# Kernel optimization log

Hardware: AMD Instinct MI355X
Metric: run time of the kernel (lower is better)

Reference implementation:

```python
import jax, jax.numpy as jnp
import numpy as np

N_NODES = 50000
N_EDGES = 500000


def setup_inputs() -> dict:
    key = jax.random.key(0)
    ks = jax.random.split(key, 24)
    p = {}
    p['x_feat'] = jax.random.normal(ks[0], (N_NODES, 24), dtype=jnp.float32)
    p['edge_index'] = jax.random.randint(ks[1], (2, N_EDGES), 0, N_NODES)
    p['edge_attr'] = jax.random.uniform(ks[2], (N_EDGES, 16), dtype=jnp.float32)
    def lin(k, fan_in, shape):
        b = 1.0 / np.sqrt(fan_in)
        return jax.random.uniform(k, shape, jnp.float32, -b, b)
    # group-0 input projection: 24 -> 32
    p['lin_prep_W'] = lin(ks[3], 24, (24, 32)); p['lin_prep_b'] = lin(ks[4], 24, (32,))
    # prep tube: 32 -> 16
    p['tube_W'] = lin(ks[5], 32, (32, 16)); p['tube_b'] = lin(ks[6], 32, (16,))
    # shared edge-attr trunk: 16 -> 32 -> 16
    p['edge_W1'] = lin(ks[7], 16, (16, 32)); p['edge_b1'] = lin(ks[8], 16, (32,))
    p['edge_W2'] = lin(ks[9], 32, (32, 16)); p['edge_b2'] = lin(ks[10], 32, (16,))
    # conv1: in=16, out=8 per aggr (mean, max, add)
    p['conv1_edge_W'] = lin(ks[11], 16, (3, 16, 16 * 8)); p['conv1_edge_b'] = lin(ks[12], 16, (3, 16 * 8))
    p['conv1_root_W'] = lin(ks[13], 16, (3, 16, 8)); p['conv1_bias'] = lin(ks[14], 16, (3, 8))
    # conv2: in=24, out=8 per aggr
    p['conv2_edge_W'] = lin(ks[15], 16, (3, 16, 24 * 8)); p['conv2_edge_b'] = lin(ks[16], 16, (3, 24 * 8))
    p['conv2_root_W'] = lin(ks[17], 24, (3, 24, 8)); p['conv2_bias'] = lin(ks[18], 24, (3, 8))
    # output head: 24 -> 2
    p['out_W'] = lin(ks[19], 24, (24, 2)); p['out_b'] = lin(ks[20], 24, (2,))
    return p


def _nnconv(x, e_repr, src, dst, edge_W, edge_b, root_W, bias, n_nodes):
    # x: [N, in]; e_repr: [E, 16]; edge_W: [3, 16, in*out]
    d_in = x.shape[1]
    x_src = x[src]  # [E, in]
    deg = jax.ops.segment_sum(jnp.ones_like(src, dtype=x.dtype), dst, num_segments=n_nodes)  # [N]
    outs = []
    for a, aggr in enumerate(('mean', 'max', 'add')):
        W_e = (e_repr @ edge_W[a] + edge_b[a]).reshape(e_repr.shape[0], d_in, -1)  # [E, in, out]
        msg = jnp.einsum('ei,eio->eo', x_src, W_e)  # [E, out]
        if aggr == 'add':
            agg = jax.ops.segment_sum(msg, dst, num_segments=n_nodes)
        elif aggr == 'mean':
            agg = jax.ops.segment_sum(msg, dst, num_segments=n_nodes) / jnp.maximum(deg, 1.0)[:, None]
        else:
            agg = jax.ops.segment_max(msg, dst, num_segments=n_nodes)
            agg = jnp.where(deg[:, None] > 0, agg, 0.0)  # no-neighbor nodes -> 0
        outs.append(agg + x @ root_W[a] + bias[a])
    return jax.nn.relu(jnp.concatenate(outs, axis=1))  # [N, 3*out]


def reference(x_feat, edge_index, edge_attr, lin_prep_W, lin_prep_b, tube_W, tube_b,
              edge_W1, edge_b1, edge_W2, edge_b2,
              conv1_edge_W, conv1_edge_b, conv1_root_W, conv1_bias,
              conv2_edge_W, conv2_edge_b, conv2_root_W, conv2_bias,
              out_W, out_b):
    n_nodes = x_feat.shape[0]
    src, dst = edge_index[0], edge_index[1]
    # node prep: group projection + tube (relu acts, dropout=0 -> identity)
    x = jax.nn.relu(x_feat @ lin_prep_W + lin_prep_b)       # [N, 32]
    x = jax.nn.relu(x @ tube_W + tube_b)                    # [N, 16]
    # shared edge-attr trunk (last activation = sigmoid), computed once
    e = jax.nn.relu(edge_attr @ edge_W1 + edge_b1)
    e_repr = jax.nn.sigmoid(e @ edge_W2 + edge_b2)          # [E, 16]
    # hop 1 and hop 2 of edge-conditioned NNConv with mean/max/add aggregators
    x = _nnconv(x, e_repr, src, dst, conv1_edge_W, conv1_edge_b, conv1_root_W, conv1_bias, n_nodes)  # [N, 24]
    x = _nnconv(x, e_repr, src, dst, conv2_edge_W, conv2_edge_b, conv2_root_W, conv2_bias, n_nodes)  # [N, 24]
    logits = x @ out_W + out_b                              # [N, 2]
    scores = jax.nn.softmax(logits, axis=1)
    return (logits, scores)
```

## Files before the change

### kernel.cpp

```cpp
#include <hip/hip_runtime.h>

#define BS 256

__device__ __forceinline__ unsigned short f2bf(float f) {
    unsigned x = __float_as_uint(f);
    return (unsigned short)((x + 0x7fffu + ((x >> 16) & 1u)) >> 16);
}
__device__ __forceinline__ void unpack8(uint4 v, float* d) {
    d[0] = __uint_as_float(v.x << 16); d[1] = __uint_as_float(v.x & 0xFFFF0000u);
    d[2] = __uint_as_float(v.y << 16); d[3] = __uint_as_float(v.y & 0xFFFF0000u);
    d[4] = __uint_as_float(v.z << 16); d[5] = __uint_as_float(v.z & 0xFFFF0000u);
    d[6] = __uint_as_float(v.w << 16); d[7] = __uint_as_float(v.w & 0xFFFF0000u);
}
__device__ __forceinline__ uint4 pack8bf(const float* r) {
    unsigned w[4];
#pragma unroll
    for (int j = 0; j < 4; j++)
        w[j] = (unsigned)f2bf(r[2 * j]) | ((unsigned)f2bf(r[2 * j + 1]) << 16);
    return make_uint4(w[0], w[1], w[2], w[3]);
}
__device__ __forceinline__ void st24bf(unsigned short* p, const float* r) {
    uint4* q = (uint4*)p;
    q[0] = pack8bf(r);
    q[1] = pack8bf(r + 8);
    q[2] = pack8bf(r + 16);
}

__global__ void prep_kernel(const float* __restrict__ xf,
                            const float* __restrict__ W1, const float* __restrict__ b1,
                            const float* __restrict__ W2, const float* __restrict__ b2,
                            float* __restrict__ x16, int N)
{
    int n = blockIdx.x * blockDim.x + threadIdx.x;
    bool valid = n < N;
    int nn = valid ? n : 0;
    float a[24];
#pragma unroll
    for (int i = 0; i < 24; i += 4)
        *(float4*)(a + i) = *(const float4*)(xf + (size_t)nn * 24 + i);
    float h[32];
#pragma unroll
    for (int j = 0; j < 32; j++) {
        float s = b1[j];
#pragma unroll
        for (int i = 0; i < 24; i++) s = fmaf(a[i], W1[i * 32 + j], s);
        h[j] = fmaxf(s, 0.f);
    }
    if (!valid) return;
#pragma unroll
    for (int j = 0; j < 16; j++) {
        float s = b2[j];
#pragma unroll
        for (int i = 0; i < 32; i++) s = fmaf(h[i], W2[i * 16 + j], s);
        x16[(size_t)n * 16 + j] = fmaxf(s, 0.f);
    }
}

__global__ void degjj_kernel(const int* __restrict__ srcA, const int* __restrict__ dstA,
                             int* __restrict__ cntS, int* __restrict__ cntD,
                             int* __restrict__ jS, int* __restrict__ jD, int E)
{
    int e = blockIdx.x * blockDim.x + threadIdx.x;
    if (e < E) {
        jS[e] = atomicAdd(&cntS[srcA[e]], 1);
        jD[e] = atomicAdd(&cntD[dstA[e]], 1);
    }
}
__global__ void offsets2_kernel(const int* __restrict__ cntS, const int* __restrict__ cntD,
                                int* __restrict__ offsS, int* __restrict__ offsD,
                                int* __restrict__ cursS, int* __restrict__ cursD, int N)
{
    int n = blockIdx.x * blockDim.x + threadIdx.x;
    int lane = threadIdx.x & 63;
    bool valid = n < N;
    int dS = valid ? cntS[n] : 0;
    int dD = valid ? cntD[n] : 0;
    int sS = dS, sD = dD;
#pragma unroll
    for (int o = 1; o < 64; o <<= 1) {
        int tS = __shfl_up(sS, o);
        int tD = __shfl_up(sD, o);
        if (lane >= o) { sS += tS; sD += tD; }
    }
    int totS = __shfl(sS, 63);
    int totD = __shfl(sD, 63);
    int baseS = 0, baseD = 0;
    if (lane == 63) {
        baseS = atomicAdd(cursS, totS);
        baseD = atomicAdd(cursD, totD);
    }
    baseS = __shfl(baseS, 63);
    baseD = __shfl(baseD, 63);
    if (valid) {
        offsS[n] = baseS + sS - dS;
        offsD[n] = baseD + sD - dD;
    }
}

__global__ __launch_bounds__(BS) void er_fill_kernel(
    const int* __restrict__ srcA, const int* __restrict__ dstA,
    const int* __restrict__ jS, const int* __restrict__ jD,
    const int* __restrict__ offsS, const int* __restrict__ offsD,
    const float* __restrict__ eattr,
    const float* __restrict__ eW1, const float* __restrict__ eb1,
    const float* __restrict__ eW2, const float* __restrict__ eb2,
    uint2* __restrict__ spq, unsigned short* __restrict__ er_s, int E)
{
    int e = blockIdx.x * BS + threadIdx.x;
    if (e >= E) return;
    int s = srcA[e], d = dstA[e];
    int p = offsS[s] + jS[e];
    int q = offsD[d] + jD[e];
    spq[p] = make_uint2((unsigned)s, (unsigned)q);

    float ea[16];
#pragma unroll
    for (int i = 0; i < 16; i += 4)
        *(float4*)(ea + i) = *(const float4*)(eattr + (size_t)e * 16 + i);
    float h[32];
#pragma unroll
    for (int j = 0; j < 32; j++) {
        float t = eb1[j];
#pragma unroll
        for (int i = 0; i < 16; i++) t = fmaf(ea[i], eW1[i * 32 + j], t);
        h[j] = fmaxf(t, 0.f);
    }
    float er[16];
#pragma unroll
    for (int j = 0; j < 16; j++) {
        float t = eb2[j];
#pragma unroll
        for (int i = 0; i < 32; i++) t = fmaf(h[i], eW2[i * 16 + j], t);
        er[j] = 1.f / (1.f + __expf(-t));
    }
    uint4* qo = (uint4*)(er_s + (size_t)p * 16);
    qo[0] = pack8bf(er);
    qo[1] = pack8bf(er + 8);
}

template <int IN>
__global__ __launch_bounds__(BS) void ynode_kernel(const float* __restrict__ x,
                                                   const float* __restrict__ W,
                                                   const float* __restrict__ B,
                                                   const float* __restrict__ RW,
                                                   const float* __restrict__ RB,
                                                   unsigned short* __restrict__ Y,
                                                   float* __restrict__ root, int N)
{
    int n = blockIdx.x * BS + threadIdx.x;
    int k = blockIdx.y;
    bool valid = n < N;
    int nn = valid ? n : 0;
    float xv[IN];
#pragma unroll
    for (int i = 0; i < IN; i += 4)
        *(float4*)(xv + i) = *(const float4*)(x + (size_t)nn * IN + i);

    float r[24];
#pragma unroll
    for (int j = 0; j < 24; j++) r[j] = 0.f;

    if (k < 16) {
        const float* w = W + (size_t)k * (IN * 8);
#pragma unroll
        for (int a = 0; a < 3; a++) {
            const float* wa = w + (size_t)a * (16 * IN * 8);
#pragma unroll
            for (int i = 0; i < IN; i++) {
                float xi = xv[i];
#pragma unroll
                for (int o = 0; o < 8; o++)
                    r[a * 8 + o] = fmaf(xi, wa[i * 8 + o], r[a * 8 + o]);
            }
        }
        if (valid) st24bf(Y + ((size_t)k * N + n) * 24, r);
    } else if (k == 16) {
#pragma unroll
        for (int a = 0; a < 3; a++) {
            const float* ba = B + (size_t)a * (IN * 8);
#pragma unroll
            for (int i = 0; i < IN; i++) {
                float xi = xv[i];
#pragma unroll
                for (int o = 0; o < 8; o++)
                    r[a * 8 + o] = fmaf(xi, ba[i * 8 + o], r[a * 8 + o]);
            }
        }
        if (valid) st24bf(Y + ((size_t)16 * N + n) * 24, r);
    } else {
#pragma unroll
        for (int j = 0; j < 24; j++) r[j] = RB[j];
#pragma unroll
        for (int a = 0; a < 3; a++) {
            const float* wa = RW + (size_t)a * (IN * 8);
#pragma unroll
            for (int i = 0; i < IN; i++) {
                float xi = xv[i];
#pragma unroll
                for (int o = 0; o < 8; o++)
                    r[a * 8 + o] = fmaf(xi, wa[i * 8 + o], r[a * 8 + o]);
            }
        }
        if (valid) {
            float* pr = root + (size_t)n * 24;
#pragma unroll
            for (int j = 0; j < 24; j += 4)
                *(float4*)(pr + j) = make_float4(r[j], r[j + 1], r[j + 2], r[j + 3]);
        }
    }
}

__global__ __launch_bounds__(BS) void msg_kernel(
    const uint2* __restrict__ spq,
    const unsigned short* __restrict__ er_s,
    const unsigned short* __restrict__ Y,
    unsigned short* __restrict__ msg16,
    int N, int E)
{
    int tid = blockIdx.x * BS + threadIdx.x;
    int p = tid / 3;
    int j = tid - p * 3;
    if (p >= E) return;

    uint2 sq = spq[p];

    float er[16];
    {
        const uint4* eu = (const uint4*)(er_s + (size_t)p * 16);
        unpack8(eu[0], er);
        unpack8(eu[1], er + 8);
    }

    const unsigned short* yb = Y + (size_t)sq.x * 24 + j * 8;
    size_t kstride = (size_t)N * 24;

    float acc[8];
    unpack8(*(const uint4*)(yb + 16 * kstride), acc);
#pragma unroll
    for (int k = 0; k < 16; k++) {
        float t[8];
        unpack8(*(const uint4*)(yb + (size_t)k * kstride), t);
        float ek = er[k];
#pragma unroll
        for (int o = 0; o < 8; o++) acc[o] = fmaf(ek, t[o], acc[o]);
    }
    *(uint4*)(msg16 + (size_t)sq.y * 24 + j * 8) = pack8bf(acc);
}

__global__ __launch_bounds__(BS) void gather_kernel(
    const unsigned short* __restrict__ msg16,
    const int* __restrict__ offs,
    const int* __restrict__ degi,
    const float* __restrict__ root,
    float* __restrict__ out, int N)
{
    int n = (blockIdx.x * BS + threadIdx.x) >> 6;
    if (n >= N) return;
    int lane = threadIdx.x & 63;
    int c = lane & 3;
    int r = lane >> 2;

    int off = offs[n];
    int d = degi[n];

    float s[8], m[8];
#pragma unroll
    for (int o = 0; o < 8; o++) { s[o] = 0.f; m[o] = -3.402823466e38f; }

    if (c < 3) {
        const unsigned short* base = msg16 + (size_t)off * 24 + c * 8;
        for (int j = r; j < d; j += 16) {
            uint4 v = *(const uint4*)(base + (size_t)j * 24);
            float t[8];
            unpack8(v, t);
#pragma unroll
            for (int o = 0; o < 8; o++) {
                s[o] += t[o];
                m[o] = fmaxf(m[o], t[o]);
            }
        }
    }
#pragma unroll
    for (int mask = 4; mask < 64; mask <<= 1) {
#pragma unroll
        for (int o = 0; o < 8; o++) {
            s[o] += __shfl_xor(s[o], mask);
            m[o] = fmaxf(m[o], __shfl_xor(m[o], mask));
        }
    }
    if (lane >= 3) return;

    float inv = 1.f / fmaxf((float)d, 1.f);
    const float* pr = root + (size_t)n * 24 + c * 8;
    float4 r0 = *(const float4*)(pr);
    float4 r1 = *(const float4*)(pr + 4);
    float rb[8] = {r0.x, r0.y, r0.z, r0.w, r1.x, r1.y, r1.z, r1.w};
    float rr[8];
#pragma unroll
    for (int o = 0; o < 8; o++) {
        float agg = (c == 0) ? s[o] * inv
                  : (c == 1) ? ((d > 0) ? m[o] : 0.f)
                  : s[o];
        rr[o] = fmaxf(rb[o] + agg, 0.f);
    }
    float* po = out + (size_t)n * 24 + c * 8;
    *(float4*)(po)     = make_float4(rr[0], rr[1], rr[2], rr[3]);
    *(float4*)(po + 4) = make_float4(rr[4], rr[5], rr[6], rr[7]);
}

__global__ void head_kernel(const float* __restrict__ x, const float* __restrict__ W,
                            const float* __restrict__ b, float* __restrict__ out, int N)
{
    int n = blockIdx.x * blockDim.x + threadIdx.x;
    if (n >= N) return;
    float l0 = b[0], l1 = b[1];
#pragma unroll
    for (int i = 0; i < 24; i++) {
        float xi = x[(size_t)n * 24 + i];
        l0 = fmaf(xi, W[i * 2 + 0], l0);
        l1 = fmaf(xi, W[i * 2 + 1], l1);
    }
    out[2 * (size_t)n + 0] = l0;
    out[2 * (size_t)n + 1] = l1;
    float mx = fmaxf(l0, l1);
    float e0 = __expf(l0 - mx), e1 = __expf(l1 - mx);
    float sm = e0 + e1;
    out[2 * (size_t)N + 2 * (size_t)n + 0] = e0 / sm;
    out[2 * (size_t)N + 2 * (size_t)n + 1] = e1 / sm;
}

extern "C" void kernel_launch(void* const* d_in, const int* in_sizes, int n_in,
                              void* d_out, int out_size, void* d_ws, size_t ws_size,
                              hipStream_t stream)
{
    const float* x_feat = (const float*)d_in[0];
    const int*   eidx   = (const int*)d_in[1];
    const float* eattr  = (const float*)d_in[2];
    const float* lpW = (const float*)d_in[3];
    const float* lpb = (const float*)d_in[4];
    const float* tW  = (const float*)d_in[5];
    const float* tb  = (const float*)d_in[6];
    const float* eW1 = (const float*)d_in[7];
    const float* eb1 = (const float*)d_in[8];
    const float* eW2 = (const float*)d_in[9];
    const float* eb2 = (const float*)d_in[10];
    const float* c1W = (const float*)d_in[11];
    const float* c1B = (const float*)d_in[12];
    const float* c1R = (const float*)d_in[13];
    const float* c1b = (const float*)d_in[14];
    const float* c2W = (const float*)d_in[15];
    const float* c2B = (const float*)d_in[16];
    const float* c2R = (const float*)d_in[17];
    const float* c2b = (const float*)d_in[18];
    const float* oW  = (const float*)d_in[19];
    const float* ob  = (const float*)d_in[20];

    int N = in_sizes[0] / 24;
    int E = in_sizes[1] / 2;
    const int* srcA = eidx;
    const int* dstA = eidx + E;

    char* wsb = (char*)d_ws;
    size_t off = 0;
    auto alloc = [&](size_t bytes) {
        off = (off + 255) & ~(size_t)255;
        void* p = wsb + off;
        off += bytes;
        return p;
    };
    unsigned short* Y     = (unsigned short*)alloc((size_t)17 * N * 24 * 2);
    unsigned short* msg16 = (unsigned short*)alloc((size_t)E * 24 * 2);
    unsigned short* er_s  = (unsigned short*)alloc((size_t)E * 16 * 2);
    float* root = (float*)alloc((size_t)N * 24 * 4);
    float* x16  = (float*)alloc((size_t)N * 16 * 4);
    float* x24a = (float*)alloc((size_t)N * 24 * 4);
    float* x24b = (float*)alloc((size_t)N * 24 * 4);
    int* ibase  = (int*)alloc(((size_t)2 * N + 2) * 4);
    int* cntS = ibase;
    int* cntD = ibase + N;
    int* cursS = ibase + 2 * N;
    int* cursD = ibase + 2 * N + 1;
    int* offsS = (int*)alloc((size_t)N * 4);
    int* offsD = (int*)alloc((size_t)N * 4);
    int* jS    = (int*)alloc((size_t)E * 4);
    int* jD    = (int*)alloc((size_t)E * 4);
    uint2* spq = (uint2*)alloc((size_t)E * 8);

    dim3 blk(BS);
    int nb_nodes = (N + BS - 1) / BS;
    int nb_edges = (E + BS - 1) / BS;
    int nb_msg   = (3 * E + BS - 1) / BS;
    int nb_gath  = ((size_t)N * 64 + BS - 1) / BS;
    dim3 ygrid(nb_nodes, 18);

    hipMemsetAsync(ibase, 0, (2 * (size_t)N + 2) * 4, stream);

    prep_kernel<<<nb_nodes, blk, 0, stream>>>(x_feat, lpW, lpb, tW, tb, x16, N);

    degjj_kernel<<<nb_edges, blk, 0, stream>>>(srcA, dstA, cntS, cntD, jS, jD, E);
    offsets2_kernel<<<nb_nodes, blk, 0, stream>>>(cntS, cntD, offsS, offsD, cursS, cursD, N);
    er_fill_kernel<<<nb_edges, blk, 0, stream>>>(srcA, dstA, jS, jD, offsS, offsD,
                                                 eattr, eW1, eb1, eW2, eb2, spq, er_s, E);

    ynode_kernel<16><<<ygrid, blk, 0, stream>>>(x16, c1W, c1B, c1R, c1b, Y, root, N);
    msg_kernel<<<nb_msg, blk, 0, stream>>>(spq, er_s, Y, msg16, N, E);
    gather_kernel<<<nb_gath, blk, 0, stream>>>(msg16, offsD, cntD, root, x24a, N);

    ynode_kernel<24><<<ygrid, blk, 0, stream>>>(x24a, c2W, c2B, c2R, c2b, Y, root, N);
    msg_kernel<<<nb_msg, blk, 0, stream>>>(spq, er_s, Y, msg16, N, E);
    gather_kernel<<<nb_gath, blk, 0, stream>>>(msg16, offsD, cntD, root, x24b, N);

    head_kernel<<<nb_nodes, blk, 0, stream>>>(x24b, oW, ob, (float*)d_out, N);
}
```

Measured before the change: 286.9 us.

## Stage ynode weights in LDS, process two nodes per thread, pad msg rows to 32

The ynode kernel now loads its 24xIN weight slice into shared memory once per block and has each thread compute two nodes, so every weight read feeds twice as many FMAs and half as many blocks are launched. It also replaces the three branch-specific loops with one unified loop. Separately, message rows are padded from 24 to 32 bf16 values (64 bytes) so each row is 64-byte aligned in msg_kernel and gather_kernel, at the cost of more buffer memory and an extra zero-store per edge.

```diff
diff --git a/kernel.cpp b/kernel.cpp
--- a/kernel.cpp
+++ b/kernel.cpp
@@ -147,65 +147,70 @@
                                                    unsigned short* __restrict__ Y,
                                                    float* __restrict__ root, int N)
 {
-    int n = blockIdx.x * BS + threadIdx.x;
+    __shared__ float w_lds[IN * 24];
+    int t = threadIdx.x;
     int k = blockIdx.y;
-    bool valid = n < N;
-    int nn = valid ? n : 0;
-    float xv[IN];
-#pragma unroll
-    for (int i = 0; i < IN; i += 4)
-        *(float4*)(xv + i) = *(const float4*)(x + (size_t)nn * IN + i);
-
-    float r[24];
-#pragma unroll
-    for (int j = 0; j < 24; j++) r[j] = 0.f;
-
-    if (k < 16) {
-        const float* w = W + (size_t)k * (IN * 8);
-#pragma unroll
-        for (int a = 0; a < 3; a++) {
-            const float* wa = w + (size_t)a * (16 * IN * 8);
-#pragma unroll
-            for (int i = 0; i < IN; i++) {
-                float xi = xv[i];
-#pragma unroll
-                for (int o = 0; o < 8; o++)
-                    r[a * 8 + o] = fmaf(xi, wa[i * 8 + o], r[a * 8 + o]);
-            }
+
+    for (int idx = t; idx < IN * 24; idx += BS) {
+        int i = idx / 24;
+        int j = idx - i * 24;
+        int a = j >> 3, o = j & 7;
+        float v;
+        if (k < 16)       v = W[(((size_t)a * 16 + k) * IN + i) * 8 + o];
+        else if (k == 16) v = B[((size_t)a * IN + i) * 8 + o];
+        else              v = RW[((size_t)a * IN + i) * 8 + o];
+        w_lds[idx] = v;
+    }
+    __syncthreads();
+
+    int n0 = blockIdx.x * (BS * 2) + t;
+    int n1 = n0 + BS;
+    bool v0 = n0 < N, v1 = n1 < N;
+    int m0 = v0 ? n0 : 0, m1 = v1 ? n1 : 0;
+
+    float xa[IN], xb[IN];
+#pragma unroll
+    for (int i = 0; i < IN; i += 4) {
+        *(float4*)(xa + i) = *(const float4*)(x + (size_t)m0 * IN + i);
+        *(float4*)(xb + i) = *(const float4*)(x + (size_t)m1 * IN + i);
+    }
+
+    float ra[24], rb[24];
+    if (k == 17) {
+#pragma unroll
+        for (int j = 0; j < 24; j++) { ra[j] = RB[j]; rb[j] = ra[j]; }
+    } else {
+#pragma unroll
+        for (int j = 0; j < 24; j++) { ra[j] = 0.f; rb[j] = 0.f; }
+    }
+
+#pragma unroll
+    for (int i = 0; i < IN; i++) {
+        float x0 = xa[i], x1 = xb[i];
+        const float* wr = w_lds + i * 24;
+#pragma unroll
+        for (int j = 0; j < 24; j++) {
+            float w = wr[j];
+            ra[j] = fmaf(x0, w, ra[j]);
+            rb[j] = fmaf(x1, w, rb[j]);
         }
-        if (valid) st24bf(Y + ((size_t)k * N + n) * 24, r);
-    } else if (k == 16) {
-#pragma unroll
-        for (int a = 0; a < 3; a++) {
-            const float* ba = B + (size_t)a * (IN * 8);
-#pragma unroll
-            for (int i = 0; i < IN; i++) {
-                float xi = xv[i];
-#pragma unroll
-                for (int o = 0; o < 8; o++)
-                    r[a * 8 + o] = fmaf(xi, ba[i * 8 + o], r[a * 8 + o]);
-            }
+    }
+
+    if (k < 17) {
+        if (v0) st24bf(Y + ((size_t)k * N + n0) * 24, ra);
+        if (v1) st24bf(Y + ((size_t)k * N + n1) * 24, rb);
+    } else {
+        if (v0) {
+            float* pr = root + (size_t)n0 * 24;
+#pragma unroll
+            for (int j = 0; j < 24; j += 4)
+                *(float4*)(pr + j) = make_float4(ra[j], ra[j+1], ra[j+2], ra[j+3]);
         }
-        if (valid) st24bf(Y + ((size_t)16 * N + n) * 24, r);
-    } else {
-#pragma unroll
-        for (int j = 0; j < 24; j++) r[j] = RB[j];
-#pragma unroll
-        for (int a = 0; a < 3; a++) {
-            const float* wa = RW + (size_t)a * (IN * 8);
-#pragma unroll
-            for (int i = 0; i < IN; i++) {
-                float xi = xv[i];
-#pragma unroll
-                for (int o = 0; o < 8; o++)
-                    r[a * 8 + o] = fmaf(xi, wa[i * 8 + o], r[a * 8 + o]);
-            }
-        }
-        if (valid) {
-            float* pr = root + (size_t)n * 24;
+        if (v1) {
+            float* pr = root + (size_t)n1 * 24;
 #pragma unroll
             for (int j = 0; j < 24; j += 4)
-                *(float4*)(pr + j) = make_float4(r[j], r[j + 1], r[j + 2], r[j + 3]);
+                *(float4*)(pr + j) = make_float4(rb[j], rb[j+1], rb[j+2], rb[j+3]);
         }
     }
 }
@@ -244,7 +249,9 @@
 #pragma unroll
         for (int o = 0; o < 8; o++) acc[o] = fmaf(ek, t[o], acc[o]);
     }
-    *(uint4*)(msg16 + (size_t)sq.y * 24 + j * 8) = pack8bf(acc);
+    unsigned short* mrow = msg16 + (size_t)sq.y * 32;
+    *(uint4*)(mrow + j * 8) = pack8bf(acc);
+    if (j == 0) *(uint4*)(mrow + 24) = make_uint4(0, 0, 0, 0);
 }
 
 __global__ __launch_bounds__(BS) void gather_kernel(
@@ -268,9 +275,9 @@
     for (int o = 0; o < 8; o++) { s[o] = 0.f; m[o] = -3.402823466e38f; }
 
     if (c < 3) {
-        const unsigned short* base = msg16 + (size_t)off * 24 + c * 8;
+        const unsigned short* base = msg16 + (size_t)off * 32 + c * 8;
         for (int j = r; j < d; j += 16) {
-            uint4 v = *(const uint4*)(base + (size_t)j * 24);
+            uint4 v = *(const uint4*)(base + (size_t)j * 32);
             float t[8];
             unpack8(v, t);
 #pragma unroll
@@ -369,7 +376,7 @@
         return p;
     };
     unsigned short* Y     = (unsigned short*)alloc((size_t)17 * N * 24 * 2);
-    unsigned short* msg16 = (unsigned short*)alloc((size_t)E * 24 * 2);
+    unsigned short* msg16 = (unsigned short*)alloc((size_t)E * 32 * 2);
     unsigned short* er_s  = (unsigned short*)alloc((size_t)E * 16 * 2);
     float* root = (float*)alloc((size_t)N * 24 * 4);
     float* x16  = (float*)alloc((size_t)N * 16 * 4);
@@ -391,7 +398,8 @@
     int nb_edges = (E + BS - 1) / BS;
     int nb_msg   = (3 * E + BS - 1) / BS;
     int nb_gath  = ((size_t)N * 64 + BS - 1) / BS;
-    dim3 ygrid(nb_nodes, 18);
+    int nb_ypair = (N + BS * 2 - 1) / (BS * 2);
+    dim3 ygrid(nb_ypair, 18);
 
     hipMemsetAsync(ibase, 0, (2 * (size_t)N + 2) * 4, stream);
 
```

After: 276.3 us. -3.7%, faster.
